# Kernel tuning notes

Hardware: AMD Instinct MI355X
Metric: run time of the kernel (lower is better)

## Reference

```python
import jax, jax.numpy as jnp
import numpy as np

N_WG = 256                 # waveguides per side
N_TOTAL = N_WG * N_WG      # 65536 field points
NNZ = 16 * N_TOTAL         # ~16 couplings per waveguide (Knn-banded)
PROP_DIS = 1.0


def setup_inputs() -> dict:
    key = jax.random.key(0)
    k1, k2, k3, k4, k5 = jax.random.split(key, 5)
    row_idx = jax.random.randint(k1, (NNZ,), 0, N_TOTAL, dtype=jnp.int32)
    col_idx = jax.random.randint(k2, (NNZ,), 0, N_TOTAL, dtype=jnp.int32)
    # small coupling values so the explicit Euler scheme stays stable
    A_vals = jax.random.normal(k3, (NNZ,), dtype=jnp.float32) * 0.01
    Ur0 = jax.random.normal(k4, (N_TOTAL, 1), dtype=jnp.float32)
    Ui0 = jax.random.normal(k5, (N_TOTAL, 1), dtype=jnp.float32)
    return {"A_vals": A_vals, "row_idx": row_idx, "col_idx": col_idx,
            "Ur0": Ur0, "Ui0": Ui0, "Euler_steps": 16}


def reference(A_vals, row_idx, col_idx, Ur0, Ui0, Euler_steps):
    """Euler propagation of a complex field U under sparse coupling A:
       dU/dz = i * A @ U  ->  Ur' = Ur - dz*A@Ui ; Ui' = Ui + dz*A@Ur.
       Matches gen_Euler_with_backward_devs.forward (single device block)."""
    dz = PROP_DIS / Euler_steps

    def spmm(x):  # sparse COO matmul: [n, n] @ [n, 1]
        return jax.ops.segment_sum(A_vals[:, None] * x[col_idx], row_idx,
                                   num_segments=N_TOTAL)

    def step(carry, _):
        Ur, Ui = carry
        Ur1 = Ur - dz * spmm(Ui)
        Ui1 = Ui + dz * spmm(Ur)
        return (Ur1, Ui1), None

    (Ur, Ui), _ = jax.lax.scan(step, (Ur0, Ui0), None, length=Euler_steps)
    return Ur + 1j * Ui
```

## Files before the change

### kernel.cpp

```cpp
#include <hip/hip_runtime.h>

#define N_TOTAL 65536
#define NNZ (16 * N_TOTAL)
#define EULER_STEPS 16
#define SLOTS 48
#define TB 256
#define P 256
#define PROWS (N_TOTAL / P)
#define CHUNK 1024
#define NCHUNK (NNZ / CHUNK)
#define PCAP 4608


__global__ __launch_bounds__(TB) void hist_kernel(
    const int* __restrict__ row_idx, int* __restrict__ hist) {
  __shared__ int h[P];
  const int b = blockIdx.x, t = threadIdx.x;
  h[t] = 0;
  __syncthreads();
  const int base = b * CHUNK;
  for (int i = t; i < CHUNK; i += TB)
    atomicAdd(&h[row_idx[base + i] >> 8], 1);
  __syncthreads();
  hist[b * P + t] = h[t];
}

__global__ __launch_bounds__(1024) void scan_kernel(
    const int* __restrict__ hist, int* __restrict__ cursor,
    int* __restrict__ partcnt) {
  __shared__ int s[1024];
  const int p = blockIdx.x, t = threadIdx.x;
  int v = hist[t * P + p];
  s[t] = v;
  __syncthreads();
  for (int off = 1; off < 1024; off <<= 1) {
    int x = (t >= off) ? s[t - off] : 0;
    __syncthreads();
    s[t] += x;
    __syncthreads();
  }
  cursor[t * P + p] = s[t] - v;
  if (t == 1023) partcnt[p] = s[t];
}

__global__ __launch_bounds__(TB) void scatter_kernel(
    const float* __restrict__ A_vals, const int* __restrict__ row_idx,
    const int* __restrict__ col_idx, const int* __restrict__ cursor,
    uint2* __restrict__ staged) {
  __shared__ int cur[P];
  const int b = blockIdx.x, t = threadIdx.x;
  cur[t] = cursor[b * P + t];
  __syncthreads();
  const int base = b * CHUNK;
  for (int i = t; i < CHUNK; i += TB) {
    int e = base + i;
    int r = row_idx[e];
    int p = r >> 8;
    int pos = atomicAdd(&cur[p], 1);
    if (pos < PCAP)
      staged[p * PCAP + pos] =
          make_uint2((unsigned)col_idx[e] | ((unsigned)(r & 255) << 16),
                     __float_as_uint(A_vals[e]));
  }
}

__global__ __launch_bounds__(512) void build_step1_kernel(
    const uint2* __restrict__ staged, const int* __restrict__ partcnt,
    int* __restrict__ cntg, unsigned* __restrict__ entries,
    const float* __restrict__ Ur0, const float* __restrict__ Ui0,
    float2* __restrict__ Unew, float dz) {
  __shared__ unsigned ell[PROWS * SLOTS];
  __shared__ int cnt[PROWS];
  const int p = blockIdx.x, t = threadIdx.x;
  for (int r = t; r < PROWS; r += 512) cnt[r] = 0;
  __syncthreads();
  int pc = partcnt[p];
  if (pc > PCAP) pc = PCAP;
  const uint2* sbase = staged + p * PCAP;
  for (int i = t; i < pc; i += 512) {
    uint2 el = sbase[i];
    int r = (el.x >> 16) & 255;
    int slot = atomicAdd(&cnt[r], 1);
    if (slot < SLOTS) {
      unsigned bv = el.y;
      unsigned rb = (bv + 0x7FFFu + ((bv >> 16) & 1u)) & 0xFFFF0000u;
      ell[r * SLOTS + slot] = (el.x & 0xFFFFu) | rb;
    }
  }
  __syncthreads();
  const int rowbase = p * PROWS;
  for (int idx = t; idx < PROWS * SLOTS; idx += 512)
    entries[rowbase * SLOTS + idx] = ell[idx];
  for (int r = t; r < PROWS; r += 512) cntg[rowbase + r] = cnt[r];
  const int lr = t >> 1, l = t & 1;
  const int row = rowbase + lr;
  int c = cnt[lr];
  if (c > SLOTS) c = SLOTS;
  float sR = 0.0f, sI = 0.0f;
  for (int s = l; s < c; s += 2) {
    unsigned e = ell[lr * SLOTS + s];
    float a = __uint_as_float(e & 0xFFFF0000u);
    int col = (int)(e & 0xFFFFu);
    sR += a * Ur0[col];
    sI += a * Ui0[col];
  }
  sR += __shfl_xor(sR, 1);
  sI += __shfl_xor(sI, 1);
  if (l == 0)
    Unew[row] = make_float2(Ur0[row] - dz * sI, Ui0[row] + dz * sR);
}

__global__ __launch_bounds__(TB) void step_mid_kernel(
    const int* __restrict__ cnt, const unsigned* __restrict__ entries,
    const float2* __restrict__ Uold, float2* __restrict__ Unew, float dz) {
  int tid = blockIdx.x * blockDim.x + threadIdx.x;
  int row = tid >> 3, l = tid & 7;
  int c = cnt[row];
  if (c > SLOTS) c = SLOTS;
  const unsigned* base = entries + row * SLOTS;
  float sR = 0.0f, sI = 0.0f;
  for (int k = 2 * l; k < c; k += 16) {
    uint2 p = *(const uint2*)(base + k);
    {
      float a = __uint_as_float(p.x & 0xFFFF0000u);
      float2 u = Uold[p.x & 0xFFFFu];
      sR += a * u.x;
      sI += a * u.y;
    }
    if (k + 1 < c) {
      float a = __uint_as_float(p.y & 0xFFFF0000u);
      float2 u = Uold[p.y & 0xFFFFu];
      sR += a * u.x;
      sI += a * u.y;
    }
  }
  sR += __shfl_xor(sR, 1); sI += __shfl_xor(sI, 1);
  sR += __shfl_xor(sR, 2); sI += __shfl_xor(sI, 2);
  sR += __shfl_xor(sR, 4); sI += __shfl_xor(sI, 4);
  if (l == 0) {
    float2 u = Uold[row];
    Unew[row] = make_float2(u.x - dz * sI, u.y + dz * sR);
  }
}

__global__ __launch_bounds__(TB) void step_final_kernel(
    const int* __restrict__ cnt, const unsigned* __restrict__ entries,
    const float2* __restrict__ Uold, float* __restrict__ UrOut,
    float* __restrict__ UiOut, float dz) {
  int tid = blockIdx.x * blockDim.x + threadIdx.x;
  int row = tid >> 3, l = tid & 7;
  int c = cnt[row];
  if (c > SLOTS) c = SLOTS;
  const unsigned* base = entries + row * SLOTS;
  float sR = 0.0f, sI = 0.0f;
  for (int k = 2 * l; k < c; k += 16) {
    uint2 p = *(const uint2*)(base + k);
    {
      float a = __uint_as_float(p.x & 0xFFFF0000u);
      float2 u = Uold[p.x & 0xFFFFu];
      sR += a * u.x;
      sI += a * u.y;
    }
    if (k + 1 < c) {
      float a = __uint_as_float(p.y & 0xFFFF0000u);
      float2 u = Uold[p.y & 0xFFFFu];
      sR += a * u.x;
      sI += a * u.y;
    }
  }
  sR += __shfl_xor(sR, 1); sI += __shfl_xor(sI, 1);
  sR += __shfl_xor(sR, 2); sI += __shfl_xor(sI, 2);
  sR += __shfl_xor(sR, 4); sI += __shfl_xor(sI, 4);
  if (l == 0) {
    float2 u = Uold[row];
    UrOut[row] = u.x - dz * sI;
    UiOut[row] = u.y + dz * sR;
  }
}

extern "C" void kernel_launch(void* const* d_in, const int* in_sizes, int n_in,
                              void* d_out, int out_size, void* d_ws,
                              size_t ws_size, hipStream_t stream) {
  const float* A_vals  = (const float*)d_in[0];
  const int*   row_idx = (const int*)d_in[1];
  const int*   col_idx = (const int*)d_in[2];
  const float* Ur0     = (const float*)d_in[3];
  const float* Ui0     = (const float*)d_in[4];

  char* ws = (char*)d_ws;
  float2*   bufA    = (float2*)ws;
  float2*   bufB    = bufA + N_TOTAL;
  int*      cntg    = (int*)(bufB + N_TOTAL);
  unsigned* entries = (unsigned*)(cntg + N_TOTAL);
  int*      hist    = (int*)(entries + N_TOTAL * SLOTS);
  int*      cursor  = hist + NCHUNK * P;
  int*      partcnt = cursor + NCHUNK * P;
  uint2*    staged  = (uint2*)(partcnt + P);

  float* UrOut = (float*)d_out;
  float* UiOut = UrOut + N_TOTAL;
  const float dz = 1.0f / (float)EULER_STEPS;
  const int gridN8 = (8 * N_TOTAL) / TB;

  hist_kernel<<<NCHUNK, TB, 0, stream>>>(row_idx, hist);
  scan_kernel<<<P, 1024, 0, stream>>>(hist, cursor, partcnt);
  scatter_kernel<<<NCHUNK, TB, 0, stream>>>(A_vals, row_idx, col_idx, cursor,
                                            staged);
  build_step1_kernel<<<P, 512, 0, stream>>>(staged, partcnt, cntg, entries,
                                            Ur0, Ui0, bufB, dz);

  for (int s = 1; s < EULER_STEPS - 1; ++s) {
    const float2* src = (s & 1) ? bufB : bufA;
    float2*       dst = (s & 1) ? bufA : bufB;
    step_mid_kernel<<<gridN8, TB, 0, stream>>>(cntg, entries, src, dst, dz);
  }
  step_final_kernel<<<gridN8, TB, 0, stream>>>(cntg, entries, bufB, UrOut,
                                               UiOut, dz);
}
```

Measured before the change: 221.3 us.

## Drop histogram and scan passes by staging into fixed per-chunk bucket slots

Removes the histogram and prefix-scan kernels. The scatter kernel now writes each chunk's entries into a fixed-capacity (24) slot region per (partition, chunk) and records per-chunk counts. The build kernel then walks those segments, one thread per chunk. This cuts two launches and a pass over row_idx, but the build loop becomes serial per thread with scattered reads, and entries past the per-chunk cap are silently dropped.

```diff
diff --git a/kernel.cpp b/kernel.cpp
--- a/kernel.cpp
+++ b/kernel.cpp
@@ -9,47 +9,16 @@
 #define PROWS (N_TOTAL / P)
 #define CHUNK 1024
 #define NCHUNK (NNZ / CHUNK)
-#define PCAP 4608
+#define SCAP 24
 
-
-__global__ __launch_bounds__(TB) void hist_kernel(
-    const int* __restrict__ row_idx, int* __restrict__ hist) {
-  __shared__ int h[P];
-  const int b = blockIdx.x, t = threadIdx.x;
-  h[t] = 0;
-  __syncthreads();
-  const int base = b * CHUNK;
-  for (int i = t; i < CHUNK; i += TB)
-    atomicAdd(&h[row_idx[base + i] >> 8], 1);
-  __syncthreads();
-  hist[b * P + t] = h[t];
-}
-
-__global__ __launch_bounds__(1024) void scan_kernel(
-    const int* __restrict__ hist, int* __restrict__ cursor,
-    int* __restrict__ partcnt) {
-  __shared__ int s[1024];
-  const int p = blockIdx.x, t = threadIdx.x;
-  int v = hist[t * P + p];
-  s[t] = v;
-  __syncthreads();
-  for (int off = 1; off < 1024; off <<= 1) {
-    int x = (t >= off) ? s[t - off] : 0;
-    __syncthreads();
-    s[t] += x;
-    __syncthreads();
-  }
-  cursor[t * P + p] = s[t] - v;
-  if (t == 1023) partcnt[p] = s[t];
-}
 
 __global__ __launch_bounds__(TB) void scatter_kernel(
     const float* __restrict__ A_vals, const int* __restrict__ row_idx,
-    const int* __restrict__ col_idx, const int* __restrict__ cursor,
+    const int* __restrict__ col_idx, int* __restrict__ hist_t,
     uint2* __restrict__ staged) {
   __shared__ int cur[P];
   const int b = blockIdx.x, t = threadIdx.x;
-  cur[t] = cursor[b * P + t];
+  cur[t] = 0;
   __syncthreads();
   const int base = b * CHUNK;
   for (int i = t; i < CHUNK; i += TB) {
@@ -57,41 +26,50 @@
     int r = row_idx[e];
     int p = r >> 8;
     int pos = atomicAdd(&cur[p], 1);
-    if (pos < PCAP)
-      staged[p * PCAP + pos] =
+    if (pos < SCAP)
+      staged[(size_t)(p * NCHUNK + b) * SCAP + pos] =
           make_uint2((unsigned)col_idx[e] | ((unsigned)(r & 255) << 16),
                      __float_as_uint(A_vals[e]));
   }
+  __syncthreads();
+  int c = cur[t];
+  hist_t[t * NCHUNK + b] = (c > SCAP) ? SCAP : c;
 }
 
 __global__ __launch_bounds__(512) void build_step1_kernel(
-    const uint2* __restrict__ staged, const int* __restrict__ partcnt,
+    const uint2* __restrict__ staged, const int* __restrict__ hist_t,
     int* __restrict__ cntg, unsigned* __restrict__ entries,
     const float* __restrict__ Ur0, const float* __restrict__ Ui0,
     float2* __restrict__ Unew, float dz) {
   __shared__ unsigned ell[PROWS * SLOTS];
   __shared__ int cnt[PROWS];
+  __shared__ int hcnt[NCHUNK];
   const int p = blockIdx.x, t = threadIdx.x;
+  for (int i = t; i < NCHUNK; i += 512) hcnt[i] = hist_t[p * NCHUNK + i];
   for (int r = t; r < PROWS; r += 512) cnt[r] = 0;
   __syncthreads();
-  int pc = partcnt[p];
-  if (pc > PCAP) pc = PCAP;
-  const uint2* sbase = staged + p * PCAP;
-  for (int i = t; i < pc; i += 512) {
-    uint2 el = sbase[i];
-    int r = (el.x >> 16) & 255;
-    int slot = atomicAdd(&cnt[r], 1);
-    if (slot < SLOTS) {
-      unsigned bv = el.y;
-      unsigned rb = (bv + 0x7FFFu + ((bv >> 16) & 1u)) & 0xFFFF0000u;
-      ell[r * SLOTS + slot] = (el.x & 0xFFFFu) | rb;
+  for (int chunk = t; chunk < NCHUNK; chunk += 512) {
+    int c = hcnt[chunk];
+    const uint2* seg = staged + (size_t)(p * NCHUNK + chunk) * SCAP;
+    for (int i = 0; i < c; ++i) {
+      uint2 el = seg[i];
+      int r = (el.x >> 16) & 255;
+      int slot = atomicAdd(&cnt[r], 1);
+      if (slot < SLOTS) {
+        unsigned bv = el.y;
+        unsigned rb = (bv + 0x7FFFu + ((bv >> 16) & 1u)) & 0xFFFF0000u;
+        ell[r * SLOTS + slot] = (el.x & 0xFFFFu) | rb;
+      }
     }
   }
   __syncthreads();
   const int rowbase = p * PROWS;
   for (int idx = t; idx < PROWS * SLOTS; idx += 512)
     entries[rowbase * SLOTS + idx] = ell[idx];
-  for (int r = t; r < PROWS; r += 512) cntg[rowbase + r] = cnt[r];
+  for (int r = t; r < PROWS; r += 512) {
+    int c = cnt[r];
+    cntg[rowbase + r] = (c > SLOTS) ? SLOTS : c;
+  }
   const int lr = t >> 1, l = t & 1;
   const int row = rowbase + lr;
   int c = cnt[lr];
@@ -192,21 +170,17 @@
   float2*   bufB    = bufA + N_TOTAL;
   int*      cntg    = (int*)(bufB + N_TOTAL);
   unsigned* entries = (unsigned*)(cntg + N_TOTAL);
-  int*      hist    = (int*)(entries + N_TOTAL * SLOTS);
-  int*      cursor  = hist + NCHUNK * P;
-  int*      partcnt = cursor + NCHUNK * P;
-  uint2*    staged  = (uint2*)(partcnt + P);
+  int*      hist_t  = (int*)(entries + (size_t)N_TOTAL * SLOTS);
+  uint2*    staged  = (uint2*)(hist_t + P * NCHUNK);
 
   float* UrOut = (float*)d_out;
   float* UiOut = UrOut + N_TOTAL;
   const float dz = 1.0f / (float)EULER_STEPS;
   const int gridN8 = (8 * N_TOTAL) / TB;
 
-  hist_kernel<<<NCHUNK, TB, 0, stream>>>(row_idx, hist);
-  scan_kernel<<<P, 1024, 0, stream>>>(hist, cursor, partcnt);
-  scatter_kernel<<<NCHUNK, TB, 0, stream>>>(A_vals, row_idx, col_idx, cursor,
+  scatter_kernel<<<NCHUNK, TB, 0, stream>>>(A_vals, row_idx, col_idx, hist_t,
                                             staged);
-  build_step1_kernel<<<P, 512, 0, stream>>>(staged, partcnt, cntg, entries,
+  build_step1_kernel<<<P, 512, 0, stream>>>(staged, hist_t, cntg, entries,
                                             Ur0, Ui0, bufB, dz);
 
   for (int s = 1; s < EULER_STEPS - 1; ++s) {
```

New measurement: 218.3 us. About the same (-1.3%).
